# Optimization experiments

Measured on AMD Instinct MI355X. Metric: run time of the kernel, lower is better.

## Reference

```python
import jax, jax.numpy as jnp
import numpy as np

N = 50000
E = 800000
D = 128  # input_dim = hidden_dim = output_dim
N_LAYERS = 3


def _graph_conv(x, src, dst, edge_weight, w_rel, b_rel, w_root):
    # PyG GraphConv (aggr='add'):
    #   out = lin_rel( sum_{j in N(i)} edge_weight_ij * x_j ) + lin_root(x_i)
    msg = x[src] * edge_weight[:, None]                      # [E, D_in]
    agg = jax.ops.segment_sum(msg, dst, num_segments=x.shape[0])  # [N, D_in]
    return agg @ w_rel + b_rel + x @ w_root                  # [N, D_out]


def setup_inputs() -> dict:
    key = jax.random.key(0)
    ks = jax.random.split(key, 4 + 3 * N_LAYERS)
    x = jax.random.normal(ks[0], (N, D), dtype=jnp.float32)
    edge_index = jax.random.randint(ks[1], (2, E), 0, N, dtype=jnp.int32)
    edge_attr = jax.random.uniform(ks[2], (E,), dtype=jnp.float32)
    scale = 1.0 / np.sqrt(D)
    inp = {"x": x, "edge_index": edge_index, "edge_attr": edge_attr}
    for l in range(N_LAYERS):
        inp[f"w_rel{l}"] = jax.random.normal(ks[3 + 3 * l], (D, D), dtype=jnp.float32) * scale
        inp[f"b_rel{l}"] = jnp.zeros((D,), dtype=jnp.float32)
        inp[f"w_root{l}"] = jax.random.normal(ks[4 + 3 * l], (D, D), dtype=jnp.float32) * scale
    return inp


def reference(x, edge_index, edge_attr,
              w_rel0, b_rel0, w_root0,
              w_rel1, b_rel1, w_root1,
              w_rel2, b_rel2, w_root2):
    src, dst = edge_index[0], edge_index[1]
    params = [(w_rel0, b_rel0, w_root0), (w_rel1, b_rel1, w_root1), (w_rel2, b_rel2, w_root2)]
    h = x
    for w_rel, b_rel, w_root in params[:-1]:
        h = _graph_conv(h, src, dst, edge_attr, w_rel, b_rel, w_root)
        h = jax.nn.relu(h)  # dropout p=0.0 -> identity
    w_rel, b_rel, w_root = params[-1]
    return _graph_conv(h, src, dst, edge_attr, w_rel, b_rel, w_root)
```

## Files before the change

kernel.cpp:

```cpp
#include <hip/hip_runtime.h>
#include <hip/hip_bf16.h>
#include <hip/hip_fp16.h>

#define N_NODES 50000
#define N_EDGES 800000
#define DIM 128

#define NBUCK 391
#define BCAP  2816
#define CHUNK 2048
#define BSLACK 384

#define CVT_BLOCKS 12500

#define LDSROW 136

typedef float floatx4 __attribute__((ext_vector_type(4)));
typedef float floatx2 __attribute__((ext_vector_type(2)));
typedef short shortx8 __attribute__((ext_vector_type(8)));

__device__ __forceinline__ unsigned short f2bf(float f) {
    union { float f; unsigned int u; } c; c.f = f;
    unsigned int u = c.u;
    unsigned int r = (u + 0x7FFFu + ((u >> 16) & 1u)) >> 16;
    return (unsigned short)r;
}
__device__ __forceinline__ unsigned char f2fp8(float f) {
    unsigned int p = __builtin_amdgcn_cvt_pk_fp8_f32(f, f, 0u, false);
    return (unsigned char)(p & 0xFFu);
}

__global__ __launch_bounds__(256)
void prep_kernel(const float* __restrict__ x, unsigned short* __restrict__ X,
                 unsigned char* __restrict__ X8,
                 const float* __restrict__ wr0, const float* __restrict__ wt0,
                 const float* __restrict__ wr1, const float* __restrict__ wt1,
                 const float* __restrict__ wr2, const float* __restrict__ wt2,
                 unsigned short* __restrict__ Wp, int* __restrict__ bcursor) {
    int b = blockIdx.x;
    if (b < CVT_BLOCKS) {
        int i = (b * 256 + threadIdx.x) * 2;
        float2 xv = *(const float2*)(x + i);
        *(unsigned int*)(X + i) =
            (unsigned int)f2bf(xv.x) | ((unsigned int)f2bf(xv.y) << 16);
        unsigned int p8 = __builtin_amdgcn_cvt_pk_fp8_f32(xv.x, xv.y, 0u, false);
        *(unsigned short*)(X8 + i) = (unsigned short)(p8 & 0xFFFFu);
    } else if (b == CVT_BLOCKS) {
        for (int i = threadIdx.x; i < NBUCK; i += 256) bcursor[i] = 0;
    } else {
        int id = (b - CVT_BLOCKS - 1) * 256 + threadIdx.x;
        int layer = id >> 15;
        int rem = id & 32767;
        int j  = rem & 7;
        int L  = (rem >> 3) & 63;
        int ct = (rem >> 9) & 7;
        int t  = rem >> 12;
        int k = t * 32 + (L >> 4) * 8 + j;
        int c = ct * 16 + (L & 15);
        const float* wr = (layer == 0) ? wr0 : (layer == 1) ? wr1 : wr2;
        const float* wt = (layer == 0) ? wt0 : (layer == 1) ? wt1 : wt2;
        float v = (k < 128) ? wr[k * 128 + c] : wt[(k - 128) * 128 + c];
        Wp[id] = f2bf(v);
    }
}

__global__ __launch_bounds__(1024)
void partition_kernel(const int* __restrict__ src, const int* __restrict__ dst,
                      const float* __restrict__ ew,
                      int* __restrict__ bcursor, int2* __restrict__ bstage, int e) {
    __shared__ int2 stage[CHUNK];
    __shared__ int cnt[NBUCK];
    __shared__ int lbase[NBUCK];
    __shared__ int gbase[NBUCK];
    __shared__ int wsum[16];
    const int tid = threadIdx.x;
    const int e0 = blockIdx.x * CHUNK;
    const int ecnt = min(CHUNK, e - e0);

    for (int i = tid; i < NBUCK; i += 1024) cnt[i] = 0;
    __syncthreads();
    for (int i = tid; i < ecnt; i += 1024)
        atomicAdd(&cnt[dst[e0 + i] >> 7], 1);
    __syncthreads();

    {
        int v = (tid < NBUCK) ? cnt[tid] : 0;
        int lane = tid & 63, wid = tid >> 6;
        int acc = v;
#pragma unroll
        for (int off = 1; off < 64; off <<= 1) {
            int t = __shfl_up(acc, off, 64);
            if (lane >= off) acc += t;
        }
        if (lane == 63) wsum[wid] = acc;
        __syncthreads();
        int wpref = 0;
        for (int w = 0; w < wid; ++w) wpref += wsum[w];
        int excl = wpref + acc - v;
        if (tid < NBUCK) {
            lbase[tid] = excl;
            gbase[tid] = atomicAdd(&bcursor[tid], v);
            cnt[tid] = 0;
        }
    }
    __syncthreads();

    for (int i = tid; i < ecnt; i += 1024) {
        int d = dst[e0 + i];
        int s = src[e0 + i];
        unsigned int hw = (unsigned int)__half_as_ushort(__float2half(ew[e0 + i]));
        int b = d >> 7;
        int pos = atomicAdd(&cnt[b], 1);
        stage[lbase[b] + pos] = make_int2((int)((hw << 16) | (unsigned int)s), d);
    }
    __syncthreads();

    for (int j = tid; j < ecnt; j += 1024) {
        int2 p = stage[j];
        int b = p.y >> 7;
        int gidx = b * BCAP + gbase[b] + (j - lbase[b]);
        bstage[gidx] = p;
    }
}

__global__ __launch_bounds__(512)
void bucket_fill_kernel(const int2* __restrict__ bstage, const int* __restrict__ bcursor,
                        int* __restrict__ row_start, int* __restrict__ row_end,
                        unsigned int* __restrict__ perm4, int n) {
    __shared__ int cnt128[128];
    __shared__ int curs[128];
    __shared__ int wsum[8];
    __shared__ int sbase, scnt;
    const int tid = threadIdx.x;
    const int b = blockIdx.x;
    const int node0 = b << 7;
    const int lane = tid & 63, wid = tid >> 6;

    {
        int v = (tid < NBUCK) ? bcursor[tid] : 0;
        int acc = v;
#pragma unroll
        for (int off = 1; off < 64; off <<= 1) {
            int t = __shfl_up(acc, off, 64);
            if (lane >= off) acc += t;
        }
        if (lane == 63) wsum[wid] = acc;
        __syncthreads();
        int wpref = 0;
        for (int w = 0; w < wid; ++w) wpref += wsum[w];
        int excl = wpref + acc - v;
        if (tid == b) { sbase = excl; scnt = v; }
    }
    __syncthreads();
    const int cntb = scnt;
    const int base = sbase + b * BSLACK;
    const int2* sp = bstage + (size_t)b * BCAP;

    if (tid < 128) cnt128[tid] = 0;
    __syncthreads();
    for (int i = tid; i < cntb; i += 512)
        atomicAdd(&cnt128[sp[i].y & 127], 1);
    __syncthreads();

    int v = (tid < 128) ? cnt128[tid] : 0;
    int pcv = (v + 3) & ~3;
    int acc = pcv;
#pragma unroll
    for (int off = 1; off < 64; off <<= 1) {
        int t = __shfl_up(acc, off, 64);
        if (lane >= off) acc += t;
    }
    if (lane == 63) wsum[wid] = acc;
    __syncthreads();
    int wpref = 0;
    for (int w = 0; w < wid; ++w) wpref += wsum[w];
    int excl = wpref + acc - pcv;
    if (tid < 128) {
        int node = node0 + tid;
        if (node < n) {
            row_start[node] = base + excl;
            row_end[node]   = base + excl + pcv;
        }
        curs[tid] = excl;
        for (int k = v; k < pcv; ++k) perm4[base + excl + k] = 0u;
    }
    __syncthreads();

    for (int i = tid; i < cntb; i += 512) {
        int2 p = sp[i];
        int pos = atomicAdd(&curs[p.y & 127], 1);
        perm4[base + pos] = (unsigned int)p.x;
    }
}

#define ACCQ(p, v) do { \
    float w_ = __half2float(__ushort_as_half((unsigned short)((p) >> 16))); \
    floatx2 W_ = (floatx2){w_, w_}; \
    floatx2 f0_ = __builtin_amdgcn_cvt_pk_f32_fp8((v).x, false); \
    floatx2 f1_ = __builtin_amdgcn_cvt_pk_f32_fp8((v).x, true);  \
    floatx2 f2_ = __builtin_amdgcn_cvt_pk_f32_fp8((v).y, false); \
    floatx2 f3_ = __builtin_amdgcn_cvt_pk_f32_fp8((v).y, true);  \
    ac[0] += W_ * f0_; ac[1] += W_ * f1_; \
    ac[2] += W_ * f2_; ac[3] += W_ * f3_; \
} while (0)

__global__ __launch_bounds__(256, 6)
void fused_layer(const unsigned short* __restrict__ h, const unsigned char* __restrict__ h8,
                 const int* __restrict__ row_start, const int* __restrict__ row_end,
                 const unsigned int* __restrict__ perm4, const unsigned short* __restrict__ Wp,
                 const float* __restrict__ bias, float* __restrict__ outF,
                 unsigned short* __restrict__ outB, unsigned char* __restrict__ outB8,
                 int relu) {
    __shared__ unsigned short Gs[16 * LDSROW];
    const int tid  = threadIdx.x;
    const int lane = tid & 63;
    const int wid  = tid >> 6;
    const int g  = lane >> 4;
    const int sl = lane & 15;
    const int rowT = blockIdx.x * 16;
    const int nodeBase = rowT + wid * 4;

    int rs = 0;
    {
        int idx = nodeBase + (lane & 3);
        if (lane < 4)      rs = row_start[idx];
        else if (lane < 8) rs = row_end[idx];
    }
    const int beg = __shfl(rs, g, 64);
    const int end = __shfl(rs, g + 4, 64);

    floatx2 ac[4];
#pragma unroll
    for (int k = 0; k < 4; ++k) ac[k] = (floatx2){0.f, 0.f};
    const unsigned char* hp8 = h8 + sl * 8;
    const bool any = beg < end;
    uint4 P = {};
    uint2 v0 = {}, v1 = {}, v2 = {}, v3 = {};
    int t = beg;
    if (any) {
        P  = *(const uint4*)(perm4 + t);
        v0 = *(const uint2*)(hp8 + (size_t)(P.x & 0xFFFFu) * DIM);
        v1 = *(const uint2*)(hp8 + (size_t)(P.y & 0xFFFFu) * DIM);
        v2 = *(const uint2*)(hp8 + (size_t)(P.z & 0xFFFFu) * DIM);
        v3 = *(const uint2*)(hp8 + (size_t)(P.w & 0xFFFFu) * DIM);
    }
    for (; t + 4 < end; t += 4) {
        uint4 Pn = *(const uint4*)(perm4 + t + 4);
        uint2 w0 = *(const uint2*)(hp8 + (size_t)(Pn.x & 0xFFFFu) * DIM);
        uint2 w1 = *(const uint2*)(hp8 + (size_t)(Pn.y & 0xFFFFu) * DIM);
        uint2 w2 = *(const uint2*)(hp8 + (size_t)(Pn.z & 0xFFFFu) * DIM);
        uint2 w3 = *(const uint2*)(hp8 + (size_t)(Pn.w & 0xFFFFu) * DIM);
        ACCQ(P.x, v0); ACCQ(P.y, v1); ACCQ(P.z, v2); ACCQ(P.w, v3);
        P = Pn;
        v0 = w0; v1 = w1; v2 = w2; v3 = w3;
    }
    if (any) { ACCQ(P.x, v0); ACCQ(P.y, v1); ACCQ(P.z, v2); ACCQ(P.w, v3); }

    {
        uint4 r;
        r.x = (unsigned int)f2bf(ac[0].x) | ((unsigned int)f2bf(ac[0].y) << 16);
        r.y = (unsigned int)f2bf(ac[1].x) | ((unsigned int)f2bf(ac[1].y) << 16);
        r.z = (unsigned int)f2bf(ac[2].x) | ((unsigned int)f2bf(ac[2].y) << 16);
        r.w = (unsigned int)f2bf(ac[3].x) | ((unsigned int)f2bf(ac[3].y) << 16);
        *(uint4*)(&Gs[(wid * 4 + g) * LDSROW + sl * 8]) = r;
    }

    floatx4 acc2[2];
#pragma unroll
    for (int ct = 0; ct < 2; ++ct) acc2[ct] = (floatx4){0.f, 0.f, 0.f, 0.f};
    const int rr = rowT + sl;
    const int ko = g * 8;
#pragma unroll
    for (int t2 = 4; t2 < 8; ++t2) {
        shortx8 a = *(const shortx8*)(h + (size_t)rr * DIM + (t2 - 4) * 32 + ko);
        const unsigned short* wp = Wp + (size_t)t2 * 4096 + (wid * 2) * 512 + lane * 8;
#pragma unroll
        for (int ct = 0; ct < 2; ++ct) {
            shortx8 b = *(const shortx8*)(wp + ct * 512);
            acc2[ct] = __builtin_amdgcn_mfma_f32_16x16x32_bf16(a, b, acc2[ct], 0, 0, 0);
        }
    }

    __syncthreads();

#pragma unroll
    for (int t2 = 0; t2 < 4; ++t2) {
        shortx8 a = *(const shortx8*)(&Gs[sl * LDSROW + t2 * 32 + ko]);
        const unsigned short* wp = Wp + (size_t)t2 * 4096 + (wid * 2) * 512 + lane * 8;
#pragma unroll
        for (int ct = 0; ct < 2; ++ct) {
            shortx8 b = *(const shortx8*)(wp + ct * 512);
            acc2[ct] = __builtin_amdgcn_mfma_f32_16x16x32_bf16(a, b, acc2[ct], 0, 0, 0);
        }
    }

#pragma unroll
    for (int ct = 0; ct < 2; ++ct) {
        int col = wid * 32 + ct * 16 + sl;
        float bv = bias[col];
#pragma unroll
        for (int i = 0; i < 4; ++i) {
            int row = rowT + g * 4 + i;
            float v = acc2[ct][i] + bv;
            if (relu) v = fmaxf(v, 0.f);
            if (outF) {
                outF[(size_t)row * DIM + col] = v;
            } else {
                outB[(size_t)row * DIM + col]  = f2bf(v);
                outB8[(size_t)row * DIM + col] = f2fp8(v);
            }
        }
    }
}

extern "C" void kernel_launch(void* const* d_in, const int* in_sizes, int n_in,
                              void* d_out, int out_size, void* d_ws, size_t ws_size,
                              hipStream_t stream) {
    const int N = N_NODES, E = N_EDGES;

    const float* x   = (const float*)d_in[0];
    const int*   ei  = (const int*)d_in[1];
    const float* ea  = (const float*)d_in[2];
    const float* wr0 = (const float*)d_in[3];
    const float* br0 = (const float*)d_in[4];
    const float* wt0 = (const float*)d_in[5];
    const float* wr1 = (const float*)d_in[6];
    const float* br1 = (const float*)d_in[7];
    const float* wt1 = (const float*)d_in[8];
    const float* wr2 = (const float*)d_in[9];
    const float* br2 = (const float*)d_in[10];
    const float* wt2 = (const float*)d_in[11];
    const int* srcI = ei;
    const int* dstI = ei + E;
    float* out = (float*)d_out;

    int2* bstage = (int2*)d_ws;
    unsigned short* X  = (unsigned short*)(bstage + (size_t)NBUCK * BCAP);
    unsigned short* H1 = X + (size_t)N * DIM;
    unsigned short* H2 = H1 + (size_t)N * DIM;
    unsigned short* Wp = H2 + (size_t)N * DIM;
    unsigned char* X8  = (unsigned char*)(Wp + 3 * 32768);
    unsigned char* H81 = X8 + (size_t)N * DIM;
    unsigned char* H82 = H81 + (size_t)N * DIM;
    unsigned int* perm4 = (unsigned int*)(H82 + (size_t)N * DIM);
    int* bcursor = (int*)(perm4 + 1000000);
    int* rowst   = bcursor + NBUCK;
    int* rowend  = rowst + N_NODES;

    prep_kernel<<<CVT_BLOCKS + 1 + 384, 256, 0, stream>>>(x, X, X8, wr0, wt0, wr1, wt1, wr2, wt2, Wp, bcursor);
    partition_kernel<<<(E + CHUNK - 1) / CHUNK, 1024, 0, stream>>>(srcI, dstI, ea, bcursor, bstage, E);
    bucket_fill_kernel<<<NBUCK, 512, 0, stream>>>(bstage, bcursor, rowst, rowend, perm4, N);

    const int fusedGrid = N / 16;

    fused_layer<<<fusedGrid, 256, 0, stream>>>(X,  X8,  rowst, rowend, perm4, Wp,         br0, nullptr, H1, H81, 1);
    fused_layer<<<fusedGrid, 256, 0, stream>>>(H1, H81, rowst, rowend, perm4, Wp + 32768, br1, nullptr, H2, H82, 1);
    fused_layer<<<fusedGrid, 256, 0, stream>>>(H2, H82, rowst, rowend, perm4, Wp + 65536, br2, out, nullptr, nullptr, 0);
}
```

Before: 211.8 us.

## Split fp8 features into column halves and unfuse aggregation from GEMM

Stores the fp8 node features as two 64-column half tables so each aggregation pass gathers from a 3.2MB table that is more likely to stay cache-resident. Each layer now runs two half-width gather kernels that write a bf16 aggregate buffer to global memory, followed by a separate MFMA GEMM kernel. The intent is better L2/MALL hit rates on the random gathers. The cost is extra kernel launches, an extra global write and read of the aggregate, and repeating the index (perm4) stream once per half.

Measured after the change: 260.3 us. 1.23x slower.

```diff
diff --git a/kernel.cpp b/kernel.cpp
--- a/kernel.cpp
+++ b/kernel.cpp
@@ -12,8 +12,6 @@
 #define BSLACK 384
 
 #define CVT_BLOCKS 12500
-
-#define LDSROW 136
 
 typedef float floatx4 __attribute__((ext_vector_type(4)));
 typedef float floatx2 __attribute__((ext_vector_type(2)));
@@ -32,7 +30,7 @@
 
 __global__ __launch_bounds__(256)
 void prep_kernel(const float* __restrict__ x, unsigned short* __restrict__ X,
-                 unsigned char* __restrict__ X8,
+                 unsigned char* __restrict__ X8a, unsigned char* __restrict__ X8b,
                  const float* __restrict__ wr0, const float* __restrict__ wt0,
                  const float* __restrict__ wr1, const float* __restrict__ wt1,
                  const float* __restrict__ wr2, const float* __restrict__ wt2,
@@ -44,7 +42,9 @@
         *(unsigned int*)(X + i) =
             (unsigned int)f2bf(xv.x) | ((unsigned int)f2bf(xv.y) << 16);
         unsigned int p8 = __builtin_amdgcn_cvt_pk_fp8_f32(xv.x, xv.y, 0u, false);
-        *(unsigned short*)(X8 + i) = (unsigned short)(p8 & 0xFFFFu);
+        int node = i >> 7, d = i & 127;
+        unsigned char* t = (d < 64) ? X8a : X8b;
+        *(unsigned short*)(t + (size_t)node * 64 + (d & 63)) = (unsigned short)(p8 & 0xFFFFu);
     } else if (b == CVT_BLOCKS) {
         for (int i = threadIdx.x; i < NBUCK; i += 256) bcursor[i] = 0;
     } else {
@@ -193,99 +193,90 @@
     }
 }
 
-#define ACCQ(p, v) do { \
+#define ACC2(p, v) do { \
     float w_ = __half2float(__ushort_as_half((unsigned short)((p) >> 16))); \
     floatx2 W_ = (floatx2){w_, w_}; \
-    floatx2 f0_ = __builtin_amdgcn_cvt_pk_f32_fp8((v).x, false); \
-    floatx2 f1_ = __builtin_amdgcn_cvt_pk_f32_fp8((v).x, true);  \
-    floatx2 f2_ = __builtin_amdgcn_cvt_pk_f32_fp8((v).y, false); \
-    floatx2 f3_ = __builtin_amdgcn_cvt_pk_f32_fp8((v).y, true);  \
-    ac[0] += W_ * f0_; ac[1] += W_ * f1_; \
-    ac[2] += W_ * f2_; ac[3] += W_ * f3_; \
+    ac0 += W_ * __builtin_amdgcn_cvt_pk_f32_fp8((v), false); \
+    ac1 += W_ * __builtin_amdgcn_cvt_pk_f32_fp8((v), true);  \
 } while (0)
 
-__global__ __launch_bounds__(256, 6)
-void fused_layer(const unsigned short* __restrict__ h, const unsigned char* __restrict__ h8,
-                 const int* __restrict__ row_start, const int* __restrict__ row_end,
-                 const unsigned int* __restrict__ perm4, const unsigned short* __restrict__ Wp,
-                 const float* __restrict__ bias, float* __restrict__ outF,
-                 unsigned short* __restrict__ outB, unsigned char* __restrict__ outB8,
-                 int relu) {
-    __shared__ unsigned short Gs[16 * LDSROW];
+__global__ __launch_bounds__(256, 8)
+void agg_half_kernel(const unsigned char* __restrict__ t8,
+                     const int* __restrict__ row_start, const int* __restrict__ row_end,
+                     const unsigned int* __restrict__ perm4,
+                     unsigned short* __restrict__ aggOut) {
+    const int tid  = threadIdx.x;
+    const int lane = tid & 63;
+    const int wid  = tid >> 6;
+    const int g  = lane >> 4;
+    const int sl = lane & 15;
+    const int nodeBase = blockIdx.x * 16 + wid * 4;
+
+    int rs = 0;
+    {
+        int idx = nodeBase + (lane & 3);
+        if (lane < 4)      rs = row_start[idx];
+        else if (lane < 8) rs = row_end[idx];
+    }
+    const int beg = __shfl(rs, g, 64);
+    const int end = __shfl(rs, g + 4, 64);
+
+    floatx2 ac0 = (floatx2){0.f, 0.f}, ac1 = (floatx2){0.f, 0.f};
+    const unsigned char* hp = t8 + sl * 4;
+    const bool any = beg < end;
+    uint4 P = {};
+    unsigned int v0 = 0, v1 = 0, v2 = 0, v3 = 0;
+    int t = beg;
+    if (any) {
+        P  = *(const uint4*)(perm4 + t);
+        v0 = *(const unsigned int*)(hp + (size_t)(P.x & 0xFFFFu) * 64);
+        v1 = *(const unsigned int*)(hp + (size_t)(P.y & 0xFFFFu) * 64);
+        v2 = *(const unsigned int*)(hp + (size_t)(P.z & 0xFFFFu) * 64);
+        v3 = *(const unsigned int*)(hp + (size_t)(P.w & 0xFFFFu) * 64);
+    }
+    for (; t + 4 < end; t += 4) {
+        uint4 Pn = *(const uint4*)(perm4 + t + 4);
+        unsigned int w0 = *(const unsigned int*)(hp + (size_t)(Pn.x & 0xFFFFu) * 64);
+        unsigned int w1 = *(const unsigned int*)(hp + (size_t)(Pn.y & 0xFFFFu) * 64);
+        unsigned int w2 = *(const unsigned int*)(hp + (size_t)(Pn.z & 0xFFFFu) * 64);
+        unsigned int w3 = *(const unsigned int*)(hp + (size_t)(Pn.w & 0xFFFFu) * 64);
+        ACC2(P.x, v0); ACC2(P.y, v1); ACC2(P.z, v2); ACC2(P.w, v3);
+        P = Pn;
+        v0 = w0; v1 = w1; v2 = w2; v3 = w3;
+    }
+    if (any) { ACC2(P.x, v0); ACC2(P.y, v1); ACC2(P.z, v2); ACC2(P.w, v3); }
+
+    uint2 r;
+    r.x = (unsigned int)f2bf(ac0.x) | ((unsigned int)f2bf(ac0.y) << 16);
+    r.y = (unsigned int)f2bf(ac1.x) | ((unsigned int)f2bf(ac1.y) << 16);
+    *(uint2*)(aggOut + (size_t)(nodeBase + g) * DIM + sl * 4) = r;
+}
+
+__global__ __launch_bounds__(256, 4)
+void gemm_layer(const unsigned short* __restrict__ h, const unsigned short* __restrict__ agg,
+                const unsigned short* __restrict__ Wp, const float* __restrict__ bias,
+                float* __restrict__ outF, unsigned short* __restrict__ outB,
+                unsigned char* __restrict__ o8a, unsigned char* __restrict__ o8b,
+                int relu) {
     const int tid  = threadIdx.x;
     const int lane = tid & 63;
     const int wid  = tid >> 6;
     const int g  = lane >> 4;
     const int sl = lane & 15;
     const int rowT = blockIdx.x * 16;
-    const int nodeBase = rowT + wid * 4;
-
-    int rs = 0;
-    {
-        int idx = nodeBase + (lane & 3);
-        if (lane < 4)      rs = row_start[idx];
-        else if (lane < 8) rs = row_end[idx];
-    }
-    const int beg = __shfl(rs, g, 64);
-    const int end = __shfl(rs, g + 4, 64);
-
-    floatx2 ac[4];
-#pragma unroll
-    for (int k = 0; k < 4; ++k) ac[k] = (floatx2){0.f, 0.f};
-    const unsigned char* hp8 = h8 + sl * 8;
-    const bool any = beg < end;
-    uint4 P = {};
-    uint2 v0 = {}, v1 = {}, v2 = {}, v3 = {};
-    int t = beg;
-    if (any) {
-        P  = *(const uint4*)(perm4 + t);
-        v0 = *(const uint2*)(hp8 + (size_t)(P.x & 0xFFFFu) * DIM);
-        v1 = *(const uint2*)(hp8 + (size_t)(P.y & 0xFFFFu) * DIM);
-        v2 = *(const uint2*)(hp8 + (size_t)(P.z & 0xFFFFu) * DIM);
-        v3 = *(const uint2*)(hp8 + (size_t)(P.w & 0xFFFFu) * DIM);
-    }
-    for (; t + 4 < end; t += 4) {
-        uint4 Pn = *(const uint4*)(perm4 + t + 4);
-        uint2 w0 = *(const uint2*)(hp8 + (size_t)(Pn.x & 0xFFFFu) * DIM);
-        uint2 w1 = *(const uint2*)(hp8 + (size_t)(Pn.y & 0xFFFFu) * DIM);
-        uint2 w2 = *(const uint2*)(hp8 + (size_t)(Pn.z & 0xFFFFu) * DIM);
-        uint2 w3 = *(const uint2*)(hp8 + (size_t)(Pn.w & 0xFFFFu) * DIM);
-        ACCQ(P.x, v0); ACCQ(P.y, v1); ACCQ(P.z, v2); ACCQ(P.w, v3);
-        P = Pn;
-        v0 = w0; v1 = w1; v2 = w2; v3 = w3;
-    }
-    if (any) { ACCQ(P.x, v0); ACCQ(P.y, v1); ACCQ(P.z, v2); ACCQ(P.w, v3); }
-
-    {
-        uint4 r;
-        r.x = (unsigned int)f2bf(ac[0].x) | ((unsigned int)f2bf(ac[0].y) << 16);
-        r.y = (unsigned int)f2bf(ac[1].x) | ((unsigned int)f2bf(ac[1].y) << 16);
-        r.z = (unsigned int)f2bf(ac[2].x) | ((unsigned int)f2bf(ac[2].y) << 16);
-        r.w = (unsigned int)f2bf(ac[3].x) | ((unsigned int)f2bf(ac[3].y) << 16);
-        *(uint4*)(&Gs[(wid * 4 + g) * LDSROW + sl * 8]) = r;
-    }
-
-    floatx4 acc2[2];
-#pragma unroll
-    for (int ct = 0; ct < 2; ++ct) acc2[ct] = (floatx4){0.f, 0.f, 0.f, 0.f};
     const int rr = rowT + sl;
     const int ko = g * 8;
-#pragma unroll
-    for (int t2 = 4; t2 < 8; ++t2) {
-        shortx8 a = *(const shortx8*)(h + (size_t)rr * DIM + (t2 - 4) * 32 + ko);
-        const unsigned short* wp = Wp + (size_t)t2 * 4096 + (wid * 2) * 512 + lane * 8;
-#pragma unroll
-        for (int ct = 0; ct < 2; ++ct) {
-            shortx8 b = *(const shortx8*)(wp + ct * 512);
-            acc2[ct] = __builtin_amdgcn_mfma_f32_16x16x32_bf16(a, b, acc2[ct], 0, 0, 0);
-        }
-    }
-
-    __syncthreads();
-
-#pragma unroll
-    for (int t2 = 0; t2 < 4; ++t2) {
-        shortx8 a = *(const shortx8*)(&Gs[sl * LDSROW + t2 * 32 + ko]);
+
+    floatx4 acc2[2];
+#pragma unroll
+    for (int ct = 0; ct < 2; ++ct) acc2[ct] = (floatx4){0.f, 0.f, 0.f, 0.f};
+
+#pragma unroll
+    for (int t2 = 0; t2 < 8; ++t2) {
+        const unsigned short* ap = (t2 < 4)
+            ? (agg + (size_t)rr * DIM + t2 * 32 + ko)
+            : (h   + (size_t)rr * DIM + (t2 - 4) * 32 + ko);
+        shortx8 a = *(const shortx8*)ap;
         const unsigned short* wp = Wp + (size_t)t2 * 4096 + (wid * 2) * 512 + lane * 8;
 #pragma unroll
         for (int ct = 0; ct < 2; ++ct) {
@@ -306,8 +297,9 @@
             if (outF) {
                 outF[(size_t)row * DIM + col] = v;
             } else {
-                outB[(size_t)row * DIM + col]  = f2bf(v);
-                outB8[(size_t)row * DIM + col] = f2fp8(v);
+                outB[(size_t)row * DIM + col] = f2bf(v);
+                unsigned char* t = (col < 64) ? o8a : o8b;
+                t[(size_t)row * 64 + (col & 63)] = f2fp8(v);
             }
         }
     }
@@ -339,21 +331,31 @@
     unsigned short* H1 = X + (size_t)N * DIM;
     unsigned short* H2 = H1 + (size_t)N * DIM;
     unsigned short* Wp = H2 + (size_t)N * DIM;
-    unsigned char* X8  = (unsigned char*)(Wp + 3 * 32768);
-    unsigned char* H81 = X8 + (size_t)N * DIM;
-    unsigned char* H82 = H81 + (size_t)N * DIM;
-    unsigned int* perm4 = (unsigned int*)(H82 + (size_t)N * DIM);
+    unsigned char* X8a  = (unsigned char*)(Wp + 3 * 32768);
+    unsigned char* X8b  = X8a  + (size_t)N * 64;
+    unsigned char* H81a = X8b  + (size_t)N * 64;
+    unsigned char* H81b = H81a + (size_t)N * 64;
+    unsigned char* H82a = H81b + (size_t)N * 64;
+    unsigned char* H82b = H82a + (size_t)N * 64;
+    unsigned short* Agg = (unsigned short*)(H82b + (size_t)N * 64);
+    unsigned int* perm4 = (unsigned int*)(Agg + (size_t)N * DIM);
     int* bcursor = (int*)(perm4 + 1000000);
     int* rowst   = bcursor + NBUCK;
     int* rowend  = rowst + N_NODES;
 
-    prep_kernel<<<CVT_BLOCKS + 1 + 384, 256, 0, stream>>>(x, X, X8, wr0, wt0, wr1, wt1, wr2, wt2, Wp, bcursor);
+    prep_kernel<<<CVT_BLOCKS + 1 + 384, 256, 0, stream>>>(x, X, X8a, X8b, wr0, wt0, wr1, wt1, wr2, wt2, Wp, bcursor);
     partition_kernel<<<(E + CHUNK - 1) / CHUNK, 1024, 0, stream>>>(srcI, dstI, ea, bcursor, bstage, E);
     bucket_fill_kernel<<<NBUCK, 512, 0, stream>>>(bstage, bcursor, rowst, rowend, perm4, N);
 
-    const int fusedGrid = N / 16;
-
-    fused_layer<<<fusedGrid, 256, 0, stream>>>(X,  X8,  rowst, rowend, perm4, Wp,         br0, nullptr, H1, H81, 1);
-    fused_layer<<<fusedGrid, 256, 0, stream>>>(H1, H81, rowst, rowend, perm4, Wp + 32768, br1, nullptr, H2, H82, 1);
-    fused_layer<<<fusedGrid, 256, 0, stream>>>(H2, H82, rowst, rowend, perm4, Wp + 65536, br2, out, nullptr, nullptr, 0);
-}
+    const int G = N / 16;
+
+    agg_half_kernel<<<G, 256, 0, stream>>>(X8a, rowst, rowend, perm4, Agg);
+    agg_half_kernel<<<G, 256, 0, stream>>>(X8b, rowst, rowend, perm4, Agg + 64);
+    gemm_layer<<<G, 256, 0, stream>>>(X, Agg, Wp, br0, nullptr, H1, H81a, H81b, 1);
+    agg_half_kernel<<<G, 256, 0, stream>>>(H81a, rowst, rowend, perm4, Agg);
+    agg_half_kernel<<<G, 256, 0, stream>>>(H81b, rowst, rowend, perm4, Agg + 64);
+    gemm_layer<<<G, 256, 0, stream>>>(H1, Agg, Wp + 32768, br1, nullptr, H2, H82a, H82b, 1);
+    agg_half_kernel<<<G, 256, 0, stream>>>(H82a, rowst, rowend, perm4, Agg);
+    agg_half_kernel<<<G, 256, 0, stream>>>(H82b, rowst, rowend, perm4, Agg + 64);
+    gemm_layer<<<G, 256, 0, stream>>>(H2, Agg, Wp + 65536, br2, out, nullptr, nullptr, nullptr, 0);
+}
```

## Make each wave own eight nodes end to end and drop block barrier

Applied to the files above, without the earlier changes.

Each wave now gathers and aggregates eight destination nodes (two per lane group, processed one after the other) and runs the full 128-column MFMA projection on them itself. The block-wide __syncthreads between the aggregation and the matmul goes away, and the block tile grows to 32 nodes. The aim is to let waves move forward independently instead of waiting on the slowest neighbour's gather. The cost is that each wave reads the whole weight matrix, and half of the 16-row MFMA work is redundant because only 8 rows are used. The launch-bounds occupancy hint also drops from 6 to 5.

After: 232.7 us. 9.9% more time.

```diff
diff --git a/kernel.cpp b/kernel.cpp
--- a/kernel.cpp
+++ b/kernel.cpp
@@ -204,110 +204,109 @@
     ac[2] += W_ * f2_; ac[3] += W_ * f3_; \
 } while (0)
 
-__global__ __launch_bounds__(256, 6)
+#define SEG(beg_, end_, lr_) do { \
+    floatx2 ac[4]; \
+    ac[0] = ac[1] = ac[2] = ac[3] = (floatx2){0.f, 0.f}; \
+    const bool any = (beg_) < (end_); \
+    uint4 P = {}; \
+    uint2 v0 = {}, v1 = {}, v2 = {}, v3 = {}; \
+    int t = (beg_); \
+    if (any) { \
+        P  = *(const uint4*)(perm4 + t); \
+        v0 = *(const uint2*)(hp8 + (size_t)(P.x & 0xFFFFu) * DIM); \
+        v1 = *(const uint2*)(hp8 + (size_t)(P.y & 0xFFFFu) * DIM); \
+        v2 = *(const uint2*)(hp8 + (size_t)(P.z & 0xFFFFu) * DIM); \
+        v3 = *(const uint2*)(hp8 + (size_t)(P.w & 0xFFFFu) * DIM); \
+    } \
+    for (; t + 4 < (end_); t += 4) { \
+        uint4 Pn = *(const uint4*)(perm4 + t + 4); \
+        uint2 w0 = *(const uint2*)(hp8 + (size_t)(Pn.x & 0xFFFFu) * DIM); \
+        uint2 w1 = *(const uint2*)(hp8 + (size_t)(Pn.y & 0xFFFFu) * DIM); \
+        uint2 w2 = *(const uint2*)(hp8 + (size_t)(Pn.z & 0xFFFFu) * DIM); \
+        uint2 w3 = *(const uint2*)(hp8 + (size_t)(Pn.w & 0xFFFFu) * DIM); \
+        ACCQ(P.x, v0); ACCQ(P.y, v1); ACCQ(P.z, v2); ACCQ(P.w, v3); \
+        P = Pn; v0 = w0; v1 = w1; v2 = w2; v3 = w3; \
+    } \
+    if (any) { ACCQ(P.x, v0); ACCQ(P.y, v1); ACCQ(P.z, v2); ACCQ(P.w, v3); } \
+    uint4 r; \
+    r.x = (unsigned int)f2bf(ac[0].x) | ((unsigned int)f2bf(ac[0].y) << 16); \
+    r.y = (unsigned int)f2bf(ac[1].x) | ((unsigned int)f2bf(ac[1].y) << 16); \
+    r.z = (unsigned int)f2bf(ac[2].x) | ((unsigned int)f2bf(ac[2].y) << 16); \
+    r.w = (unsigned int)f2bf(ac[3].x) | ((unsigned int)f2bf(ac[3].y) << 16); \
+    *(uint4*)(&Gs[(size_t)(lr_) * LDSROW + sl * 8]) = r; \
+} while (0)
+
+__global__ __launch_bounds__(256, 5)
 void fused_layer(const unsigned short* __restrict__ h, const unsigned char* __restrict__ h8,
                  const int* __restrict__ row_start, const int* __restrict__ row_end,
                  const unsigned int* __restrict__ perm4, const unsigned short* __restrict__ Wp,
                  const float* __restrict__ bias, float* __restrict__ outF,
                  unsigned short* __restrict__ outB, unsigned char* __restrict__ outB8,
                  int relu) {
-    __shared__ unsigned short Gs[16 * LDSROW];
+    __shared__ unsigned short Gs[32 * LDSROW];
     const int tid  = threadIdx.x;
     const int lane = tid & 63;
     const int wid  = tid >> 6;
     const int g  = lane >> 4;
     const int sl = lane & 15;
-    const int rowT = blockIdx.x * 16;
-    const int nodeBase = rowT + wid * 4;
+    const int waveBase = blockIdx.x * 32 + wid * 8;
+    if (waveBase >= N_NODES) return;
+    const int n0 = waveBase + g * 2;
 
     int rs = 0;
+    if (sl < 2)       rs = row_start[n0 + sl];
+    else if (sl == 2) rs = row_end[n0 + 1];
+    const int gb = g << 4;
+    const int s0 = __shfl(rs, gb + 0, 64);
+    const int s1 = __shfl(rs, gb + 1, 64);
+    const int s2 = __shfl(rs, gb + 2, 64);
+
+    const unsigned char* hp8 = h8 + sl * 8;
+    unsigned short* GsW = Gs;
     {
-        int idx = nodeBase + (lane & 3);
-        if (lane < 4)      rs = row_start[idx];
-        else if (lane < 8) rs = row_end[idx];
-    }
-    const int beg = __shfl(rs, g, 64);
-    const int end = __shfl(rs, g + 4, 64);
-
-    floatx2 ac[4];
-#pragma unroll
-    for (int k = 0; k < 4; ++k) ac[k] = (floatx2){0.f, 0.f};
-    const unsigned char* hp8 = h8 + sl * 8;
-    const bool any = beg < end;
-    uint4 P = {};
-    uint2 v0 = {}, v1 = {}, v2 = {}, v3 = {};
-    int t = beg;
-    if (any) {
-        P  = *(const uint4*)(perm4 + t);
-        v0 = *(const uint2*)(hp8 + (size_t)(P.x & 0xFFFFu) * DIM);
-        v1 = *(const uint2*)(hp8 + (size_t)(P.y & 0xFFFFu) * DIM);
-        v2 = *(const uint2*)(hp8 + (size_t)(P.z & 0xFFFFu) * DIM);
-        v3 = *(const uint2*)(hp8 + (size_t)(P.w & 0xFFFFu) * DIM);
-    }
-    for (; t + 4 < end; t += 4) {
-        uint4 Pn = *(const uint4*)(perm4 + t + 4);
-        uint2 w0 = *(const uint2*)(hp8 + (size_t)(Pn.x & 0xFFFFu) * DIM);
-        uint2 w1 = *(const uint2*)(hp8 + (size_t)(Pn.y & 0xFFFFu) * DIM);
-        uint2 w2 = *(const uint2*)(hp8 + (size_t)(Pn.z & 0xFFFFu) * DIM);
-        uint2 w3 = *(const uint2*)(hp8 + (size_t)(Pn.w & 0xFFFFu) * DIM);
-        ACCQ(P.x, v0); ACCQ(P.y, v1); ACCQ(P.z, v2); ACCQ(P.w, v3);
-        P = Pn;
-        v0 = w0; v1 = w1; v2 = w2; v3 = w3;
-    }
-    if (any) { ACCQ(P.x, v0); ACCQ(P.y, v1); ACCQ(P.z, v2); ACCQ(P.w, v3); }
-
-    {
-        uint4 r;
-        r.x = (unsigned int)f2bf(ac[0].x) | ((unsigned int)f2bf(ac[0].y) << 16);
-        r.y = (unsigned int)f2bf(ac[1].x) | ((unsigned int)f2bf(ac[1].y) << 16);
-        r.z = (unsigned int)f2bf(ac[2].x) | ((unsigned int)f2bf(ac[2].y) << 16);
-        r.w = (unsigned int)f2bf(ac[3].x) | ((unsigned int)f2bf(ac[3].y) << 16);
-        *(uint4*)(&Gs[(wid * 4 + g) * LDSROW + sl * 8]) = r;
-    }
-
-    floatx4 acc2[2];
-#pragma unroll
-    for (int ct = 0; ct < 2; ++ct) acc2[ct] = (floatx4){0.f, 0.f, 0.f, 0.f};
-    const int rr = rowT + sl;
+        const int lr0 = wid * 8 + g * 2;
+        SEG(s0, s1, lr0);
+        SEG(s1, s2, lr0 + 1);
+    }
+    (void)GsW;
+
+    floatx4 acc2[8];
+#pragma unroll
+    for (int ct = 0; ct < 8; ++ct) acc2[ct] = (floatx4){0.f, 0.f, 0.f, 0.f};
+    const int arow = wid * 8 + (sl & 7);
+    const int rr = waveBase + (sl & 7);
     const int ko = g * 8;
 #pragma unroll
-    for (int t2 = 4; t2 < 8; ++t2) {
-        shortx8 a = *(const shortx8*)(h + (size_t)rr * DIM + (t2 - 4) * 32 + ko);
-        const unsigned short* wp = Wp + (size_t)t2 * 4096 + (wid * 2) * 512 + lane * 8;
-#pragma unroll
-        for (int ct = 0; ct < 2; ++ct) {
+    for (int t2 = 0; t2 < 8; ++t2) {
+        shortx8 a;
+        if (t2 < 4)
+            a = *(const shortx8*)(&Gs[(size_t)arow * LDSROW + t2 * 32 + ko]);
+        else
+            a = *(const shortx8*)(h + (size_t)rr * DIM + (t2 - 4) * 32 + ko);
+        const unsigned short* wp = Wp + (size_t)t2 * 4096 + lane * 8;
+#pragma unroll
+        for (int ct = 0; ct < 8; ++ct) {
             shortx8 b = *(const shortx8*)(wp + ct * 512);
             acc2[ct] = __builtin_amdgcn_mfma_f32_16x16x32_bf16(a, b, acc2[ct], 0, 0, 0);
         }
     }
 
-    __syncthreads();
-
-#pragma unroll
-    for (int t2 = 0; t2 < 4; ++t2) {
-        shortx8 a = *(const shortx8*)(&Gs[sl * LDSROW + t2 * 32 + ko]);
-        const unsigned short* wp = Wp + (size_t)t2 * 4096 + (wid * 2) * 512 + lane * 8;
-#pragma unroll
-        for (int ct = 0; ct < 2; ++ct) {
-            shortx8 b = *(const shortx8*)(wp + ct * 512);
-            acc2[ct] = __builtin_amdgcn_mfma_f32_16x16x32_bf16(a, b, acc2[ct], 0, 0, 0);
-        }
-    }
-
-#pragma unroll
-    for (int ct = 0; ct < 2; ++ct) {
-        int col = wid * 32 + ct * 16 + sl;
-        float bv = bias[col];
-#pragma unroll
-        for (int i = 0; i < 4; ++i) {
-            int row = rowT + g * 4 + i;
-            float v = acc2[ct][i] + bv;
-            if (relu) v = fmaxf(v, 0.f);
-            if (outF) {
-                outF[(size_t)row * DIM + col] = v;
-            } else {
-                outB[(size_t)row * DIM + col]  = f2bf(v);
-                outB8[(size_t)row * DIM + col] = f2fp8(v);
+    if (g < 2) {
+#pragma unroll
+        for (int ct = 0; ct < 8; ++ct) {
+            int col = ct * 16 + sl;
+            float bv = bias[col];
+#pragma unroll
+            for (int i = 0; i < 4; ++i) {
+                int row = waveBase + g * 4 + i;
+                float v = acc2[ct][i] + bv;
+                if (relu) v = fmaxf(v, 0.f);
+                if (outF) {
+                    outF[(size_t)row * DIM + col] = v;
+                } else {
+                    outB[(size_t)row * DIM + col]  = f2bf(v);
+                    outB8[(size_t)row * DIM + col] = f2fp8(v);
+                }
             }
         }
     }
@@ -351,7 +350,7 @@
     partition_kernel<<<(E + CHUNK - 1) / CHUNK, 1024, 0, stream>>>(srcI, dstI, ea, bcursor, bstage, E);
     bucket_fill_kernel<<<NBUCK, 512, 0, stream>>>(bstage, bcursor, rowst, rowend, perm4, N);
 
-    const int fusedGrid = N / 16;
+    const int fusedGrid = (N + 31) / 32;
 
     fused_layer<<<fusedGrid, 256, 0, stream>>>(X,  X8,  rowst, rowend, perm4, Wp,         br0, nullptr, H1, H81, 1);
     fused_layer<<<fusedGrid, 256, 0, stream>>>(H1, H81, rowst, rowend, perm4, Wp + 32768, br1, nullptr, H2, H82, 1);
```
